# Kernel tuning notes

Hardware: AMD Instinct MI355X
Metric: run time of the kernel (lower is better)

## Reference

```python
import jax, jax.numpy as jnp
import numpy as np


def pairwise_dist(x):
    # Euclidean cdist via the expansion trick; grad-safe sqrt (0 grad at 0, like torch).
    sq = jnp.sum(x * x, axis=1)
    d2 = sq[:, None] + sq[None, :] - 2.0 * (x @ x.T)
    d2 = jnp.maximum(d2, 0.0)
    pos = d2 > 0
    return jnp.where(pos, jnp.sqrt(jnp.where(pos, d2, 1.0)), 0.0)


def knn_mask(dist, k):
    # per-row ascending sort; skip index 0 (self), take next k neighbors
    idx = jnp.argsort(dist, axis=1)[:, 1:k + 1]            # [N, k]
    n = dist.shape[0]
    return jnp.zeros_like(dist).at[jnp.arange(n)[:, None], idx].set(1.0)


def setup_inputs() -> dict:
    key = jax.random.key(0)
    k1, k2 = jax.random.split(key)
    N, D, K = 8192, 64, 12
    latent = jax.random.normal(k1, (N, D), dtype=jnp.float32)
    latent_norm = jnp.ones((), dtype=jnp.float32)
    X = jax.random.normal(k2, (N, D), dtype=jnp.float32)
    dist_X = pairwise_dist(X)
    pair_mask_X = knn_mask(dist_X, K)
    return {"latent": latent, "latent_norm": latent_norm,
            "dist_X": dist_X, "pair_mask_X": pair_mask_X, "k": K}


def reference(latent, latent_norm, dist_X, pair_mask_X, k):
    n = latent.shape[0]
    dist_Z = pairwise_dist(latent) / latent_norm
    pair_mask_Z = knn_mask(dist_Z, k)

    mask_diff = pair_mask_Z - pair_mask_X
    matched = (n * k - jnp.sum(mask_diff != 0) * 0.5) / (n * k)

    # match_edges == 'symmetric'
    sig1 = dist_X * pair_mask_X
    sig1_2 = dist_Z * pair_mask_X
    distance1_2 = jnp.sum(jnp.square(sig1 - sig1_2))
    sig2 = dist_Z * pair_mask_Z
    sig2_1 = dist_X * pair_mask_Z
    distance2_1 = jnp.sum(jnp.square(sig2_1 - sig2))
    distance = distance1_2 + distance2_1
    return (distance, matched, distance1_2, distance2_1)
```

## Files before the change

kernel.cpp:

```cpp
#include <hip/hip_runtime.h>
#include <stdint.h>

constexpr int NPTS = 8192;
constexpr int DIM  = 64;
constexpr int KNN  = 12;

constexpr int RT = 64;
constexpr int CT = 64;
constexpr int CS = 4;
constexpr int STRIPE = NPTS / CS;
constexpr int NCHUNK = STRIPE / CT;
constexpr int LSTR = 72;

constexpr unsigned long long SENTINEL = 0xFFFFFFFFFFFFFFFFull;

typedef short bf16x8 __attribute__((ext_vector_type(8)));
typedef float f32x4  __attribute__((ext_vector_type(4)));

__device__ __forceinline__ unsigned short f2bf(float x) {
  unsigned u = __float_as_uint(x);
  return (unsigned short)((u + 0x7FFFu + ((u >> 16) & 1u)) >> 16);
}
__device__ __forceinline__ float bf2f(unsigned short h) {
  return __uint_as_float(((unsigned)h) << 16);
}

__global__ __launch_bounds__(256) void init_kernel(float* out, int* ecnt) {
  int g = blockIdx.x * 256 + threadIdx.x;
  if (g < NPTS) ecnt[g] = 0;
  if (g < 4) out[g] = 0.0f;
}

__global__ __launch_bounds__(256) void conv_kernel(
    const float* __restrict__ latent, unsigned short* __restrict__ Lh,
    unsigned short* __restrict__ Ll, float* __restrict__ sq) {
  int i = blockIdx.x * 256 + threadIdx.x;
  const float4* p = reinterpret_cast<const float4*>(latent + (size_t)i * DIM);
  float s = 0.f;
#pragma unroll
  for (int t = 0; t < DIM / 4; ++t) {
    float4 v = p[t];
    s += v.x * v.x + v.y * v.y + v.z * v.z + v.w * v.w;
    ushort4 h, l;
    h.x = f2bf(v.x); l.x = f2bf(v.x - bf2f(h.x));
    h.y = f2bf(v.y); l.y = f2bf(v.y - bf2f(h.y));
    h.z = f2bf(v.z); l.z = f2bf(v.z - bf2f(h.z));
    h.w = f2bf(v.w); l.w = f2bf(v.w - bf2f(h.w));
    *reinterpret_cast<ushort4*>(Lh + (size_t)i * DIM + t * 4) = h;
    *reinterpret_cast<ushort4*>(Ll + (size_t)i * DIM + t * 4) = l;
  }
  sq[i] = s;
}

__global__ __launch_bounds__(256) void scan_mask(
    const float* __restrict__ mask_X, const float* __restrict__ dist_X,
    int* __restrict__ ecnt, int* __restrict__ ecol, float* __restrict__ edx) {
  const int total4 = NPTS * NPTS / 4;
  int stride = gridDim.x * 256;
  for (int idx4 = blockIdx.x * 256 + threadIdx.x; idx4 < total4; idx4 += stride) {
    float4 m = reinterpret_cast<const float4*>(mask_X)[idx4];
    if (m.x == 0.f && m.y == 0.f && m.z == 0.f && m.w == 0.f) continue;
    int base = idx4 * 4;
    float mv[4] = {m.x, m.y, m.z, m.w};
#pragma unroll
    for (int c = 0; c < 4; ++c) {
      if (mv[c] != 0.f) {
        int pos = base + c;
        int i = pos >> 13, j = pos & (NPTS - 1);
        int slot = atomicAdd(&ecnt[i], 1);
        if (slot < KNN) {
          ecol[i * KNN + slot] = j;
          edx[i * KNN + slot] = dist_X[pos];
        }
      }
    }
  }
}

__device__ __forceinline__ void topk_insert(unsigned long long cand,
                                            unsigned long long pk[KNN]) {
#pragma unroll
  for (int s = KNN - 1; s >= 0; --s) {
    bool belongs = cand < pk[s];
    bool shift = (s > 0) && (cand < pk[s - 1]);
    unsigned long long nv = shift ? pk[s - 1] : cand;
    if (belongs) pk[s] = nv;
  }
}

__global__ __launch_bounds__(256, 2) void dz_main(
    const unsigned short* __restrict__ Lh, const unsigned short* __restrict__ Ll,
    const float* __restrict__ sq, unsigned long long* __restrict__ topk_ws) {
  __shared__ unsigned short Ah[RT * LSTR], Al[RT * LSTR];
  __shared__ unsigned short Bh[CT * LSTR], Bl[CT * LSTR];
  __shared__ unsigned long long buf[RT * CT];
  __shared__ int   cnt[RT];
  __shared__ float thr[RT];
  __shared__ float sqA[RT];
  __shared__ float sqB[CT];

  const int tid = threadIdx.x;
  const int tile = blockIdx.x / CS;
  const int split = blockIdx.x % CS;
  const int ib = tile * RT;
  const int jb0 = split * STRIPE;

  const int wid = tid >> 6;
  const int lane = tid & 63;
  const int quad = lane >> 4;
  const int l16 = lane & 15;
  const int wr = wid >> 1;
  const int wc = wid & 1;

#pragma unroll
  for (int it = 0; it < 2; ++it) {
    int f = it * 256 + tid;
    int r = f >> 3, c = f & 7;
    const uint4* sh = reinterpret_cast<const uint4*>(Lh + (size_t)(ib + r) * DIM + c * 8);
    const uint4* sl = reinterpret_cast<const uint4*>(Ll + (size_t)(ib + r) * DIM + c * 8);
    *reinterpret_cast<uint4*>(&Ah[r * LSTR + c * 8]) = *sh;
    *reinterpret_cast<uint4*>(&Al[r * LSTR + c * 8]) = *sl;
  }
  if (tid < RT) { sqA[tid] = sq[ib + tid]; thr[tid] = 3.4e38f; }

  unsigned long long pk[KNN];
#pragma unroll
  for (int t = 0; t < KNN; ++t) pk[t] = SENTINEL;

  for (int ch = 0; ch < NCHUNK; ++ch) {
    const int jb = jb0 + ch * CT;
    __syncthreads();
#pragma unroll
    for (int it = 0; it < 2; ++it) {
      int f = it * 256 + tid;
      int r = f >> 3, c = f & 7;
      const uint4* sh = reinterpret_cast<const uint4*>(Lh + (size_t)(jb + r) * DIM + c * 8);
      const uint4* sl = reinterpret_cast<const uint4*>(Ll + (size_t)(jb + r) * DIM + c * 8);
      *reinterpret_cast<uint4*>(&Bh[r * LSTR + c * 8]) = *sh;
      *reinterpret_cast<uint4*>(&Bl[r * LSTR + c * 8]) = *sl;
    }
    if (tid < CT) sqB[tid] = sq[jb + tid];
    if (tid < RT) cnt[tid] = 0;
    __syncthreads();

    f32x4 acc[2][2];
#pragma unroll
    for (int rb = 0; rb < 2; ++rb)
#pragma unroll
      for (int cb = 0; cb < 2; ++cb) acc[rb][cb] = (f32x4){0.f, 0.f, 0.f, 0.f};

#pragma unroll
    for (int kk = 0; kk < 2; ++kk) {
      const int ko = kk * 32 + quad * 8;
      bf16x8 ah[2], al[2], bh[2], bl[2];
#pragma unroll
      for (int rb = 0; rb < 2; ++rb) {
        int row = wr * 32 + rb * 16 + l16;
        ah[rb] = *reinterpret_cast<const bf16x8*>(&Ah[row * LSTR + ko]);
        al[rb] = *reinterpret_cast<const bf16x8*>(&Al[row * LSTR + ko]);
      }
#pragma unroll
      for (int cb = 0; cb < 2; ++cb) {
        int col = wc * 32 + cb * 16 + l16;
        bh[cb] = *reinterpret_cast<const bf16x8*>(&Bh[col * LSTR + ko]);
        bl[cb] = *reinterpret_cast<const bf16x8*>(&Bl[col * LSTR + ko]);
      }
#pragma unroll
      for (int rb = 0; rb < 2; ++rb)
#pragma unroll
        for (int cb = 0; cb < 2; ++cb) {
          acc[rb][cb] = __builtin_amdgcn_mfma_f32_16x16x32_bf16(ah[rb], bh[cb], acc[rb][cb], 0, 0, 0);
          acc[rb][cb] = __builtin_amdgcn_mfma_f32_16x16x32_bf16(ah[rb], bl[cb], acc[rb][cb], 0, 0, 0);
          acc[rb][cb] = __builtin_amdgcn_mfma_f32_16x16x32_bf16(al[rb], bh[cb], acc[rb][cb], 0, 0, 0);
        }
    }

#pragma unroll
    for (int rb = 0; rb < 2; ++rb) {
      const int row0 = wr * 32 + rb * 16 + quad * 4;
#pragma unroll
      for (int r = 0; r < 4; ++r) {
        const int rl = row0 + r;
        const int gi = ib + rl;
        const float sa = sqA[rl];
        const float t_thr = thr[rl];
#pragma unroll
        for (int cb = 0; cb < 2; ++cb) {
          const int col_l = wc * 32 + cb * 16 + l16;
          const int gj = jb + col_l;
          float d2 = sa + sqB[col_l] - 2.0f * acc[rb][cb][r];
          float d2c = fmaxf(d2, 0.0f);
          if (d2c < t_thr && gj != gi) {
            int pos = atomicAdd(&cnt[rl], 1);
            buf[rl * CT + pos] =
                ((unsigned long long)__float_as_uint(d2c) << 32) | (unsigned)gj;
          }
        }
      }
    }
    __syncthreads();

    if (tid < RT) {
      int n = cnt[tid];
      for (int t = 0; t < n; ++t) {
        unsigned long long cand = buf[tid * CT + t];
        if (cand < pk[KNN - 1]) topk_insert(cand, pk);
      }
      thr[tid] = __uint_as_float((unsigned)(pk[KNN - 1] >> 32));
    }
  }

  if (tid < RT) {
    size_t base = ((size_t)(ib + tid) * CS + split) * KNN;
#pragma unroll
    for (int t = 0; t < KNN; ++t) topk_ws[base + t] = pk[t];
  }
}

__global__ __launch_bounds__(256) void sig1_kernel(
    const float* __restrict__ latent, const float* __restrict__ latent_norm,
    const int* __restrict__ ecol, const float* __restrict__ edx,
    float* __restrict__ d_out) {
  __shared__ float red[256];
  const int tid = threadIdx.x;
  const int e = blockIdx.x * 256 + tid;
  const float invnorm = 1.0f / latent_norm[0];

  int i = e / KNN;
  int j = ecol[e];
  float dx = edx[e];
  const float4* a = reinterpret_cast<const float4*>(latent + (size_t)i * DIM);
  const float4* b = reinterpret_cast<const float4*>(latent + (size_t)j * DIM);
  float d2 = 0.f;
#pragma unroll
  for (int t = 0; t < DIM / 4; ++t) {
    float4 va = a[t], vb = b[t];
    float ex = va.x - vb.x, ey = va.y - vb.y, ez = va.z - vb.z, ew = va.w - vb.w;
    d2 += ex * ex + ey * ey + ez * ez + ew * ew;
  }
  float dz = (d2 > 0.f) ? sqrtf(d2) * invnorm : 0.f;
  float diff = dx - dz;
  float acc = diff * diff;

  red[tid] = acc;
  __syncthreads();
  for (int s = 128; s > 0; s >>= 1) {
    if (tid < s) red[tid] += red[tid + s];
    __syncthreads();
  }
  if (tid == 0) {
    atomicAdd(&d_out[2], red[0]);
    atomicAdd(&d_out[0], red[0]);
  }
}

__global__ __launch_bounds__(256) void finalize_kernel(
    const float* __restrict__ latent_norm, const float* __restrict__ dist_X,
    const int* __restrict__ ecol, const unsigned long long* __restrict__ topk_ws,
    float* __restrict__ d_out) {
  __shared__ float red[256];
  const int tid = threadIdx.x;
  const int gi = blockIdx.x * 256 + tid;
  const float invnorm = 1.0f / latent_norm[0];

  unsigned long long pk[KNN];
#pragma unroll
  for (int t = 0; t < KNN; ++t) pk[t] = SENTINEL;

  const unsigned long long* src = topk_ws + (size_t)gi * CS * KNN;
  for (int t = 0; t < CS * KNN; ++t) {
    unsigned long long cand = src[t];
    if (cand < pk[KNN - 1]) topk_insert(cand, pk);
  }

  int ec[KNN];
#pragma unroll
  for (int t = 0; t < KNN; ++t) ec[t] = ecol[gi * KNN + t];

  float acc2 = 0.f, accc = 0.f;
#pragma unroll
  for (int t = 0; t < KNN; ++t) {
    int j = (int)(unsigned)(pk[t] & 0xFFFFFFFFull);
    float d2 = __uint_as_float((unsigned)(pk[t] >> 32));
    float dz = (d2 > 0.0f) ? sqrtf(d2) * invnorm : 0.0f;
    float dxv = dist_X[(size_t)gi * NPTS + j];
    float diff = dxv - dz;
    acc2 += diff * diff;
    int hit = 0;
#pragma unroll
    for (int s = 0; s < KNN; ++s) hit |= (ec[s] == j);
    accc += (float)hit;
  }

  red[tid] = acc2;
  __syncthreads();
  for (int s = 128; s > 0; s >>= 1) {
    if (tid < s) red[tid] += red[tid + s];
    __syncthreads();
  }
  float racc2 = red[0];
  __syncthreads();
  red[tid] = accc;
  __syncthreads();
  for (int s = 128; s > 0; s >>= 1) {
    if (tid < s) red[tid] += red[tid + s];
    __syncthreads();
  }
  if (tid == 0) {
    atomicAdd(&d_out[3], racc2);
    atomicAdd(&d_out[0], racc2);
    atomicAdd(&d_out[1], red[0] * (1.0f / ((float)NPTS * (float)KNN)));
  }
}

extern "C" void kernel_launch(void* const* d_in, const int* in_sizes, int n_in,
                              void* d_out, int out_size, void* d_ws,
                              size_t ws_size, hipStream_t stream) {
  const float* latent      = (const float*)d_in[0];
  const float* latent_norm = (const float*)d_in[1];
  const float* dist_X      = (const float*)d_in[2];
  const float* mask_X      = (const float*)d_in[3];
  float* out = (float*)d_out;

  char* w = (char*)d_ws;
  float*          sq   = (float*)w;                    w += NPTS * 4;
  unsigned short* Lh   = (unsigned short*)w;           w += NPTS * DIM * 2;
  unsigned short* Ll   = (unsigned short*)w;           w += NPTS * DIM * 2;
  int*            ecnt = (int*)w;                      w += NPTS * 4;
  int*            ecol = (int*)w;                      w += NPTS * KNN * 4;
  float*          edx  = (float*)w;                    w += NPTS * KNN * 4;
  unsigned long long* topk = (unsigned long long*)w;

  init_kernel<<<NPTS / 256, 256, 0, stream>>>(out, ecnt);
  conv_kernel<<<NPTS / 256, 256, 0, stream>>>(latent, Lh, Ll, sq);
  scan_mask<<<2048, 256, 0, stream>>>(mask_X, dist_X, ecnt, ecol, edx);
  dz_main<<<(NPTS / RT) * CS, 256, 0, stream>>>(Lh, Ll, sq, topk);
  sig1_kernel<<<NPTS * KNN / 256, 256, 0, stream>>>(latent, latent_norm, ecol,
                                                    edx, out);
  finalize_kernel<<<NPTS / 256, 256, 0, stream>>>(latent_norm, dist_X, ecol,
                                                  topk, out);
}
```

Before: 661.3 us.

## Fuse mask scan into distance kernel and merge init/conv and tail kernels

Folds the 256MB mask_X scan into the main distance/top-k kernel, so each workgroup streams its share of the mask with nontemporal loads, overlapped with the MFMA work. It also merges init into conv and sig1 into finalize, cutting the launch count from six to three. The A tile is now held in registers instead of LDS, the candidate buffer is split into padded float/int arrays, and barriers become a raw waitcnt+s_barrier. The cost is higher register pressure, extra atomics inside the main loop, and dist_X being gathered in the tail instead of stored during the scan.

Result: faster. 620.7 us (-6.1%).

```diff
diff --git a/kernel.cpp b/kernel.cpp
--- a/kernel.cpp
+++ b/kernel.cpp
@@ -11,11 +11,19 @@
 constexpr int STRIPE = NPTS / CS;
 constexpr int NCHUNK = STRIPE / CT;
 constexpr int LSTR = 72;
+constexpr int BSTR = 65;
+
+constexpr int NWG_DZ = (NPTS / RT) * CS;
+constexpr int TOT4   = NPTS * NPTS / 4;
+constexpr int WG4    = TOT4 / NWG_DZ;
+constexpr int CH4    = WG4 / NCHUNK;
 
 constexpr unsigned long long SENTINEL = 0xFFFFFFFFFFFFFFFFull;
 
 typedef short bf16x8 __attribute__((ext_vector_type(8)));
 typedef float f32x4  __attribute__((ext_vector_type(4)));
+
+#define WG_BARRIER() asm volatile("s_waitcnt lgkmcnt(0)\n\ts_barrier" ::: "memory")
 
 __device__ __forceinline__ unsigned short f2bf(float x) {
   unsigned u = __float_as_uint(x);
@@ -25,16 +33,13 @@
   return __uint_as_float(((unsigned)h) << 16);
 }
 
-__global__ __launch_bounds__(256) void init_kernel(float* out, int* ecnt) {
-  int g = blockIdx.x * 256 + threadIdx.x;
-  if (g < NPTS) ecnt[g] = 0;
-  if (g < 4) out[g] = 0.0f;
-}
-
-__global__ __launch_bounds__(256) void conv_kernel(
+__global__ __launch_bounds__(256) void prep_kernel(
     const float* __restrict__ latent, unsigned short* __restrict__ Lh,
-    unsigned short* __restrict__ Ll, float* __restrict__ sq) {
+    unsigned short* __restrict__ Ll, float* __restrict__ sq,
+    int* __restrict__ ecnt, float* __restrict__ out) {
   int i = blockIdx.x * 256 + threadIdx.x;
+  ecnt[i] = 0;
+  if (i < 4) out[i] = 0.0f;
   const float4* p = reinterpret_cast<const float4*>(latent + (size_t)i * DIM);
   float s = 0.f;
 #pragma unroll
@@ -52,31 +57,6 @@
   sq[i] = s;
 }
 
-__global__ __launch_bounds__(256) void scan_mask(
-    const float* __restrict__ mask_X, const float* __restrict__ dist_X,
-    int* __restrict__ ecnt, int* __restrict__ ecol, float* __restrict__ edx) {
-  const int total4 = NPTS * NPTS / 4;
-  int stride = gridDim.x * 256;
-  for (int idx4 = blockIdx.x * 256 + threadIdx.x; idx4 < total4; idx4 += stride) {
-    float4 m = reinterpret_cast<const float4*>(mask_X)[idx4];
-    if (m.x == 0.f && m.y == 0.f && m.z == 0.f && m.w == 0.f) continue;
-    int base = idx4 * 4;
-    float mv[4] = {m.x, m.y, m.z, m.w};
-#pragma unroll
-    for (int c = 0; c < 4; ++c) {
-      if (mv[c] != 0.f) {
-        int pos = base + c;
-        int i = pos >> 13, j = pos & (NPTS - 1);
-        int slot = atomicAdd(&ecnt[i], 1);
-        if (slot < KNN) {
-          ecol[i * KNN + slot] = j;
-          edx[i * KNN + slot] = dist_X[pos];
-        }
-      }
-    }
-  }
-}
-
 __device__ __forceinline__ void topk_insert(unsigned long long cand,
                                             unsigned long long pk[KNN]) {
 #pragma unroll
@@ -88,12 +68,21 @@
   }
 }
 
-__global__ __launch_bounds__(256, 2) void dz_main(
+__device__ __forceinline__ void push_edge(int pos, int* __restrict__ ecnt,
+                                          int* __restrict__ ecol) {
+  int i = pos >> 13, j = pos & (NPTS - 1);
+  int slot = atomicAdd(&ecnt[i], 1);
+  if (slot < KNN) ecol[i * KNN + slot] = j;
+}
+
+__global__ __launch_bounds__(256, 2) void main_kernel(
     const unsigned short* __restrict__ Lh, const unsigned short* __restrict__ Ll,
-    const float* __restrict__ sq, unsigned long long* __restrict__ topk_ws) {
-  __shared__ unsigned short Ah[RT * LSTR], Al[RT * LSTR];
+    const float* __restrict__ sq, unsigned long long* __restrict__ topk_ws,
+    const float* __restrict__ mask_X, int* __restrict__ ecnt,
+    int* __restrict__ ecol) {
   __shared__ unsigned short Bh[CT * LSTR], Bl[CT * LSTR];
-  __shared__ unsigned long long buf[RT * CT];
+  __shared__ float d2b[RT * BSTR];
+  __shared__ int   colb[RT * BSTR];
   __shared__ int   cnt[RT];
   __shared__ float thr[RT];
   __shared__ float sqA[RT];
@@ -112,16 +101,21 @@
   const int wr = wid >> 1;
   const int wc = wid & 1;
 
-#pragma unroll
-  for (int it = 0; it < 2; ++it) {
-    int f = it * 256 + tid;
-    int r = f >> 3, c = f & 7;
-    const uint4* sh = reinterpret_cast<const uint4*>(Lh + (size_t)(ib + r) * DIM + c * 8);
-    const uint4* sl = reinterpret_cast<const uint4*>(Ll + (size_t)(ib + r) * DIM + c * 8);
-    *reinterpret_cast<uint4*>(&Ah[r * LSTR + c * 8]) = *sh;
-    *reinterpret_cast<uint4*>(&Al[r * LSTR + c * 8]) = *sl;
+  bf16x8 ahr[2][2], alr[2][2];
+#pragma unroll
+  for (int kk = 0; kk < 2; ++kk) {
+    const int ko = kk * 32 + quad * 8;
+#pragma unroll
+    for (int rb = 0; rb < 2; ++rb) {
+      const int row = ib + wr * 32 + rb * 16 + l16;
+      ahr[kk][rb] = *reinterpret_cast<const bf16x8*>(Lh + (size_t)row * DIM + ko);
+      alr[kk][rb] = *reinterpret_cast<const bf16x8*>(Ll + (size_t)row * DIM + ko);
+    }
   }
   if (tid < RT) { sqA[tid] = sq[ib + tid]; thr[tid] = 3.4e38f; }
+
+  const f32x4* mbase = reinterpret_cast<const f32x4*>(mask_X);
+  const int wgBase4 = blockIdx.x * WG4;
 
   unsigned long long pk[KNN];
 #pragma unroll
@@ -129,19 +123,28 @@
 
   for (int ch = 0; ch < NCHUNK; ++ch) {
     const int jb = jb0 + ch * CT;
-    __syncthreads();
+    WG_BARRIER();
+
 #pragma unroll
     for (int it = 0; it < 2; ++it) {
       int f = it * 256 + tid;
       int r = f >> 3, c = f & 7;
-      const uint4* sh = reinterpret_cast<const uint4*>(Lh + (size_t)(jb + r) * DIM + c * 8);
-      const uint4* sl = reinterpret_cast<const uint4*>(Ll + (size_t)(jb + r) * DIM + c * 8);
-      *reinterpret_cast<uint4*>(&Bh[r * LSTR + c * 8]) = *sh;
-      *reinterpret_cast<uint4*>(&Bl[r * LSTR + c * 8]) = *sl;
+      uint4 vh = *reinterpret_cast<const uint4*>(Lh + (size_t)(jb + r) * DIM + c * 8);
+      uint4 vl = *reinterpret_cast<const uint4*>(Ll + (size_t)(jb + r) * DIM + c * 8);
+      *reinterpret_cast<uint4*>(&Bh[r * LSTR + c * 8]) = vh;
+      *reinterpret_cast<uint4*>(&Bl[r * LSTR + c * 8]) = vl;
     }
     if (tid < CT) sqB[tid] = sq[jb + tid];
     if (tid < RT) cnt[tid] = 0;
-    __syncthreads();
+
+    __builtin_amdgcn_sched_barrier(0);
+    f32x4 m[4];
+    const int mb = wgBase4 + ch * CH4 + tid;
+#pragma unroll
+    for (int q = 0; q < 4; ++q)
+      m[q] = __builtin_nontemporal_load(&mbase[mb + q * 256]);
+
+    WG_BARRIER();
 
     f32x4 acc[2][2];
 #pragma unroll
@@ -152,13 +155,7 @@
 #pragma unroll
     for (int kk = 0; kk < 2; ++kk) {
       const int ko = kk * 32 + quad * 8;
-      bf16x8 ah[2], al[2], bh[2], bl[2];
-#pragma unroll
-      for (int rb = 0; rb < 2; ++rb) {
-        int row = wr * 32 + rb * 16 + l16;
-        ah[rb] = *reinterpret_cast<const bf16x8*>(&Ah[row * LSTR + ko]);
-        al[rb] = *reinterpret_cast<const bf16x8*>(&Al[row * LSTR + ko]);
-      }
+      bf16x8 bh[2], bl[2];
 #pragma unroll
       for (int cb = 0; cb < 2; ++cb) {
         int col = wc * 32 + cb * 16 + l16;
@@ -169,9 +166,9 @@
       for (int rb = 0; rb < 2; ++rb)
 #pragma unroll
         for (int cb = 0; cb < 2; ++cb) {
-          acc[rb][cb] = __builtin_amdgcn_mfma_f32_16x16x32_bf16(ah[rb], bh[cb], acc[rb][cb], 0, 0, 0);
-          acc[rb][cb] = __builtin_amdgcn_mfma_f32_16x16x32_bf16(ah[rb], bl[cb], acc[rb][cb], 0, 0, 0);
-          acc[rb][cb] = __builtin_amdgcn_mfma_f32_16x16x32_bf16(al[rb], bh[cb], acc[rb][cb], 0, 0, 0);
+          acc[rb][cb] = __builtin_amdgcn_mfma_f32_16x16x32_bf16(ahr[kk][rb], bh[cb], acc[rb][cb], 0, 0, 0);
+          acc[rb][cb] = __builtin_amdgcn_mfma_f32_16x16x32_bf16(ahr[kk][rb], bl[cb], acc[rb][cb], 0, 0, 0);
+          acc[rb][cb] = __builtin_amdgcn_mfma_f32_16x16x32_bf16(alr[kk][rb], bh[cb], acc[rb][cb], 0, 0, 0);
         }
     }
 
@@ -192,22 +189,35 @@
           float d2c = fmaxf(d2, 0.0f);
           if (d2c < t_thr && gj != gi) {
             int pos = atomicAdd(&cnt[rl], 1);
-            buf[rl * CT + pos] =
-                ((unsigned long long)__float_as_uint(d2c) << 32) | (unsigned)gj;
+            d2b[rl * BSTR + pos] = d2c;
+            colb[rl * BSTR + pos] = gj;
           }
         }
       }
     }
-    __syncthreads();
+    WG_BARRIER();
 
     if (tid < RT) {
       int n = cnt[tid];
       for (int t = 0; t < n; ++t) {
-        unsigned long long cand = buf[tid * CT + t];
+        unsigned long long cand =
+            ((unsigned long long)__float_as_uint(d2b[tid * BSTR + t]) << 32) |
+            (unsigned)colb[tid * BSTR + t];
         if (cand < pk[KNN - 1]) topk_insert(cand, pk);
       }
       thr[tid] = __uint_as_float((unsigned)(pk[KNN - 1] >> 32));
     }
+
+#pragma unroll
+    for (int q = 0; q < 4; ++q) {
+      f32x4 mv = m[q];
+      if (mv[0] == 0.f && mv[1] == 0.f && mv[2] == 0.f && mv[3] == 0.f) continue;
+      const int base = (mb + q * 256) * 4;
+      if (mv[0] != 0.f) push_edge(base + 0, ecnt, ecol);
+      if (mv[1] != 0.f) push_edge(base + 1, ecnt, ecol);
+      if (mv[2] != 0.f) push_edge(base + 2, ecnt, ecol);
+      if (mv[3] != 0.f) push_edge(base + 3, ecnt, ecol);
+    }
   }
 
   if (tid < RT) {
@@ -217,99 +227,92 @@
   }
 }
 
-__global__ __launch_bounds__(256) void sig1_kernel(
+__global__ __launch_bounds__(256) void tail_kernel(
     const float* __restrict__ latent, const float* __restrict__ latent_norm,
-    const int* __restrict__ ecol, const float* __restrict__ edx,
-    float* __restrict__ d_out) {
+    const float* __restrict__ dist_X, const int* __restrict__ ecol,
+    const unsigned long long* __restrict__ topk_ws, float* __restrict__ d_out) {
   __shared__ float red[256];
   const int tid = threadIdx.x;
-  const int e = blockIdx.x * 256 + tid;
   const float invnorm = 1.0f / latent_norm[0];
 
-  int i = e / KNN;
-  int j = ecol[e];
-  float dx = edx[e];
-  const float4* a = reinterpret_cast<const float4*>(latent + (size_t)i * DIM);
-  const float4* b = reinterpret_cast<const float4*>(latent + (size_t)j * DIM);
-  float d2 = 0.f;
-#pragma unroll
-  for (int t = 0; t < DIM / 4; ++t) {
-    float4 va = a[t], vb = b[t];
-    float ex = va.x - vb.x, ey = va.y - vb.y, ez = va.z - vb.z, ew = va.w - vb.w;
-    d2 += ex * ex + ey * ey + ez * ez + ew * ew;
-  }
-  float dz = (d2 > 0.f) ? sqrtf(d2) * invnorm : 0.f;
-  float diff = dx - dz;
-  float acc = diff * diff;
-
-  red[tid] = acc;
-  __syncthreads();
-  for (int s = 128; s > 0; s >>= 1) {
-    if (tid < s) red[tid] += red[tid + s];
+  if (blockIdx.x < (NPTS * KNN / 256)) {
+    const int e = blockIdx.x * 256 + tid;
+    int i = e / KNN;
+    int j = ecol[e];
+    float dx = dist_X[(size_t)i * NPTS + j];
+    const float4* a = reinterpret_cast<const float4*>(latent + (size_t)i * DIM);
+    const float4* b = reinterpret_cast<const float4*>(latent + (size_t)j * DIM);
+    float d2 = 0.f;
+#pragma unroll
+    for (int t = 0; t < DIM / 4; ++t) {
+      float4 va = a[t], vb = b[t];
+      float ex = va.x - vb.x, ey = va.y - vb.y, ez = va.z - vb.z, ew = va.w - vb.w;
+      d2 += ex * ex + ey * ey + ez * ez + ew * ew;
+    }
+    float dz = (d2 > 0.f) ? sqrtf(d2) * invnorm : 0.f;
+    float diff = dx - dz;
+
+    red[tid] = diff * diff;
     __syncthreads();
-  }
-  if (tid == 0) {
-    atomicAdd(&d_out[2], red[0]);
-    atomicAdd(&d_out[0], red[0]);
-  }
-}
-
-__global__ __launch_bounds__(256) void finalize_kernel(
-    const float* __restrict__ latent_norm, const float* __restrict__ dist_X,
-    const int* __restrict__ ecol, const unsigned long long* __restrict__ topk_ws,
-    float* __restrict__ d_out) {
-  __shared__ float red[256];
-  const int tid = threadIdx.x;
-  const int gi = blockIdx.x * 256 + tid;
-  const float invnorm = 1.0f / latent_norm[0];
-
-  unsigned long long pk[KNN];
-#pragma unroll
-  for (int t = 0; t < KNN; ++t) pk[t] = SENTINEL;
-
-  const unsigned long long* src = topk_ws + (size_t)gi * CS * KNN;
-  for (int t = 0; t < CS * KNN; ++t) {
-    unsigned long long cand = src[t];
-    if (cand < pk[KNN - 1]) topk_insert(cand, pk);
-  }
-
-  int ec[KNN];
-#pragma unroll
-  for (int t = 0; t < KNN; ++t) ec[t] = ecol[gi * KNN + t];
-
-  float acc2 = 0.f, accc = 0.f;
-#pragma unroll
-  for (int t = 0; t < KNN; ++t) {
-    int j = (int)(unsigned)(pk[t] & 0xFFFFFFFFull);
-    float d2 = __uint_as_float((unsigned)(pk[t] >> 32));
-    float dz = (d2 > 0.0f) ? sqrtf(d2) * invnorm : 0.0f;
-    float dxv = dist_X[(size_t)gi * NPTS + j];
-    float diff = dxv - dz;
-    acc2 += diff * diff;
-    int hit = 0;
-#pragma unroll
-    for (int s = 0; s < KNN; ++s) hit |= (ec[s] == j);
-    accc += (float)hit;
-  }
-
-  red[tid] = acc2;
-  __syncthreads();
-  for (int s = 128; s > 0; s >>= 1) {
-    if (tid < s) red[tid] += red[tid + s];
+    for (int s = 128; s > 0; s >>= 1) {
+      if (tid < s) red[tid] += red[tid + s];
+      __syncthreads();
+    }
+    if (tid == 0) {
+      atomicAdd(&d_out[2], red[0]);
+      atomicAdd(&d_out[0], red[0]);
+    }
+  } else {
+    const int gi = (blockIdx.x - NPTS * KNN / 256) * 256 + tid;
+
+    unsigned long long pk[KNN];
+#pragma unroll
+    for (int t = 0; t < KNN; ++t) pk[t] = SENTINEL;
+
+    const unsigned long long* src = topk_ws + (size_t)gi * CS * KNN;
+    for (int t = 0; t < CS * KNN; ++t) {
+      unsigned long long cand = src[t];
+      if (cand < pk[KNN - 1]) topk_insert(cand, pk);
+    }
+
+    int ec[KNN];
+#pragma unroll
+    for (int t = 0; t < KNN; ++t) ec[t] = ecol[gi * KNN + t];
+
+    float acc2 = 0.f, accc = 0.f;
+#pragma unroll
+    for (int t = 0; t < KNN; ++t) {
+      int j = (int)(unsigned)(pk[t] & 0xFFFFFFFFull);
+      float d2 = __uint_as_float((unsigned)(pk[t] >> 32));
+      float dz = (d2 > 0.0f) ? sqrtf(d2) * invnorm : 0.0f;
+      float dxv = dist_X[(size_t)gi * NPTS + j];
+      float diff = dxv - dz;
+      acc2 += diff * diff;
+      int hit = 0;
+#pragma unroll
+      for (int s = 0; s < KNN; ++s) hit |= (ec[s] == j);
+      accc += (float)hit;
+    }
+
+    red[tid] = acc2;
     __syncthreads();
-  }
-  float racc2 = red[0];
-  __syncthreads();
-  red[tid] = accc;
-  __syncthreads();
-  for (int s = 128; s > 0; s >>= 1) {
-    if (tid < s) red[tid] += red[tid + s];
+    for (int s = 128; s > 0; s >>= 1) {
+      if (tid < s) red[tid] += red[tid + s];
+      __syncthreads();
+    }
+    float racc2 = red[0];
     __syncthreads();
-  }
-  if (tid == 0) {
-    atomicAdd(&d_out[3], racc2);
-    atomicAdd(&d_out[0], racc2);
-    atomicAdd(&d_out[1], red[0] * (1.0f / ((float)NPTS * (float)KNN)));
+    red[tid] = accc;
+    __syncthreads();
+    for (int s = 128; s > 0; s >>= 1) {
+      if (tid < s) red[tid] += red[tid + s];
+      __syncthreads();
+    }
+    if (tid == 0) {
+      atomicAdd(&d_out[3], racc2);
+      atomicAdd(&d_out[0], racc2);
+      atomicAdd(&d_out[1], red[0] * (1.0f / ((float)NPTS * (float)KNN)));
+    }
   }
 }
 
@@ -328,15 +331,10 @@
   unsigned short* Ll   = (unsigned short*)w;           w += NPTS * DIM * 2;
   int*            ecnt = (int*)w;                      w += NPTS * 4;
   int*            ecol = (int*)w;                      w += NPTS * KNN * 4;
-  float*          edx  = (float*)w;                    w += NPTS * KNN * 4;
   unsigned long long* topk = (unsigned long long*)w;
 
-  init_kernel<<<NPTS / 256, 256, 0, stream>>>(out, ecnt);
-  conv_kernel<<<NPTS / 256, 256, 0, stream>>>(latent, Lh, Ll, sq);
-  scan_mask<<<2048, 256, 0, stream>>>(mask_X, dist_X, ecnt, ecol, edx);
-  dz_main<<<(NPTS / RT) * CS, 256, 0, stream>>>(Lh, Ll, sq, topk);
-  sig1_kernel<<<NPTS * KNN / 256, 256, 0, stream>>>(latent, latent_norm, ecol,
-                                                    edx, out);
-  finalize_kernel<<<NPTS / 256, 256, 0, stream>>>(latent_norm, dist_X, ecol,
-                                                  topk, out);
-}
+  prep_kernel<<<NPTS / 256, 256, 0, stream>>>(latent, Lh, Ll, sq, ecnt, out);
+  main_kernel<<<NWG_DZ, 256, 0, stream>>>(Lh, Ll, sq, topk, mask_X, ecnt, ecol);
+  tail_kernel<<<NPTS * KNN / 256 + NPTS / 256, 256, 0, stream>>>(
+      latent, latent_norm, dist_X, ecol, topk, out);
+}
```
